# Kernel optimization log

Hardware: AMD Instinct MI355X
Metric: run time of the kernel (lower is better)

The kernel has to match this reference:

```python
import jax, jax.numpy as jnp
import numpy as np

HIDDEN_DIM = 64
VOCAB_SIZE = 64
NUM_SLOTS = 64
B, L = 256, 4096
EPS = 1e-5


def setup_inputs() -> dict:
    key = jax.random.key(0)
    ks = jax.random.split(key, 8)
    s = 0.02
    return {
        "seq": jax.random.randint(ks[0], (B, L), 0, VOCAB_SIZE),
        "embed": jax.random.normal(ks[1], (VOCAB_SIZE, HIDDEN_DIM), jnp.float32) * s,
        "W1": jax.random.normal(ks[2], (HIDDEN_DIM, 2 * HIDDEN_DIM), jnp.float32) * s,
        "b1": jnp.zeros((2 * HIDDEN_DIM,), jnp.float32),
        "W2": jax.random.normal(ks[3], (2 * HIDDEN_DIM, HIDDEN_DIM), jnp.float32) * s,
        "b2": jnp.zeros((HIDDEN_DIM,), jnp.float32),
        "gamma": jnp.ones((HIDDEN_DIM,), jnp.float32),
        "beta": jnp.zeros((HIDDEN_DIM,), jnp.float32),
        "Wq": jax.random.normal(ks[4], (HIDDEN_DIM, HIDDEN_DIM), jnp.float32) * s,
        "bq": jnp.zeros((HIDDEN_DIM,), jnp.float32),
        "Wo": jax.random.normal(ks[5], (HIDDEN_DIM, VOCAB_SIZE), jnp.float32) * s,
        "bo": jnp.zeros((VOCAB_SIZE,), jnp.float32),
    }


def reference(seq, embed, W1, b1, W2, b2, gamma, beta, Wq, bq, Wo, bo):
    # Encoder: embed -> FF residual -> LayerNorm
    e = embed[seq]                                   # [B, L, H]
    ff = jax.nn.relu(e @ W1 + b1) @ W2 + b2          # [B, L, H]
    h = e + ff
    mu = jnp.mean(h, axis=-1, keepdims=True)
    var = jnp.mean(jnp.square(h - mu), axis=-1, keepdims=True)
    hs = (h - mu) * jax.lax.rsqrt(var + EPS) * gamma + beta  # [B, L, H]

    # Top-k gating over content token norms
    content = hs[:, :-3, :]                          # [B, L-3, H]
    gate_scores = jnp.linalg.norm(content, axis=-1)  # [B, L-3]
    _, idx = jax.lax.top_k(gate_scores, NUM_SLOTS)   # [B, k], k == num_slots (L-3 >= k)
    slots = jnp.take_along_axis(content, idx[:, :, None], axis=1)  # [B, k, H]

    # Tiny single-query attention over gathered slots
    q = hs[:, -1, :] @ Wq + bq                       # [B, H]
    scores = jnp.einsum("bh,bkh->bk", q, slots) / jnp.sqrt(jnp.float32(HIDDEN_DIM))
    attn = jax.nn.softmax(scores, axis=-1)           # [B, k]
    ctx = jnp.einsum("bk,bkh->bh", attn, slots)      # [B, H]
    return ctx @ Wo + bo                             # [B, VOCAB]
```

## Files before the change

kernel.cpp:

```cpp
#include <hip/hip_runtime.h>
#include <math.h>

#define EPS 1e-5f


__global__ __launch_bounds__(512) void table_hist(
    const int* __restrict__ seq,
    const float* __restrict__ embed,
    const float* __restrict__ W1, const float* __restrict__ b1,
    const float* __restrict__ W2, const float* __restrict__ b2,
    const float* __restrict__ gamma, const float* __restrict__ beta,
    float* __restrict__ wsf, int* __restrict__ wsi_hist,
    int* __restrict__ wsi_tlast)
{
    const int tid = threadIdx.x;
    const int wv  = tid >> 6;
    const int ln  = tid & 63;

    if (blockIdx.x < 8) {
        const int t = blockIdx.x * 8 + wv;
        float e = embed[t * 64 + ln];

        float a0p0 = b1[ln],      a0p1 = 0.f;
        float a1p0 = b1[64 + ln], a1p1 = 0.f;
        #pragma unroll 8
        for (int j = 0; j < 64; j += 2) {
            float ej0 = __shfl(e, j);
            float ej1 = __shfl(e, j + 1);
            a0p0 = fmaf(ej0, W1[j * 128 + ln],            a0p0);
            a1p0 = fmaf(ej0, W1[j * 128 + 64 + ln],       a1p0);
            a0p1 = fmaf(ej1, (W1 + 128)[j * 128 + ln],      a0p1);
            a1p1 = fmaf(ej1, (W1 + 128)[j * 128 + 64 + ln], a1p1);
        }
        float u0 = fmaxf(a0p0 + a0p1, 0.f);
        float u1 = fmaxf(a1p0 + a1p1, 0.f);

        float hp0 = e + b2[ln], hp1 = 0.f;
        #pragma unroll 8
        for (int k = 0; k < 64; k += 2) {
            hp0 = fmaf(__shfl(u0, k),     W2[k * 64 + ln],       hp0);
            hp1 = fmaf(__shfl(u0, k + 1), W2[(k + 1) * 64 + ln], hp1);
        }
        #pragma unroll 8
        for (int k = 0; k < 64; k += 2) {
            hp0 = fmaf(__shfl(u1, k),     W2[(64 + k) * 64 + ln],     hp0);
            hp1 = fmaf(__shfl(u1, k + 1), W2[(64 + k + 1) * 64 + ln], hp1);
        }
        float h = hp0 + hp1;

        float s = h;
        #pragma unroll
        for (int off = 1; off < 64; off <<= 1) s += __shfl_xor(s, off);
        float mu = s * (1.f / 64.f);
        float d = h - mu;
        float v = d * d;
        #pragma unroll
        for (int off = 1; off < 64; off <<= 1) v += __shfl_xor(v, off);
        float rstd = rsqrtf(v * (1.f / 64.f) + EPS);
        float hs = d * rstd * gamma[ln] + beta[ln];
        wsf[t * 64 + ln] = hs;
        float ss = hs * hs;
        #pragma unroll
        for (int off = 1; off < 64; off <<= 1) ss += __shfl_xor(ss, off);
        if (ln == 0) wsf[4096 + t] = sqrtf(ss);
    } else {
        __shared__ int hist[8][64];
        const int b = blockIdx.x - 8;
        const int* row = seq + b * 4096;

        hist[wv][ln] = 0;
        int4 v0 = reinterpret_cast<const int4*>(row)[tid];
        int4 v1 = reinterpret_cast<const int4*>(row)[tid + 512];
        __syncthreads();

        atomicAdd(&hist[wv][v0.x], 1); atomicAdd(&hist[wv][v0.y], 1);
        atomicAdd(&hist[wv][v0.z], 1); atomicAdd(&hist[wv][v0.w], 1);
        atomicAdd(&hist[wv][v1.x], 1);
        if (tid != 511) {
            atomicAdd(&hist[wv][v1.y], 1);
            atomicAdd(&hist[wv][v1.z], 1);
            atomicAdd(&hist[wv][v1.w], 1);
        } else {
            wsi_tlast[b] = v1.w;
        }
        __syncthreads();

        if (tid < 64) {
            int hsum = 0;
            #pragma unroll
            for (int w = 0; w < 8; ++w) hsum += hist[w][tid];
            wsi_hist[b * 64 + tid] = hsum;
        }
    }
}

__global__ __launch_bounds__(256) void slot_epilogue(
    const float* __restrict__ Wq, const float* __restrict__ bq,
    const float* __restrict__ Wo, const float* __restrict__ bo,
    const float* __restrict__ wsf, const int* __restrict__ wsi_hist,
    const int* __restrict__ wsi_tlast,
    float* __restrict__ out)
{
    __shared__ float HS[64][65];
    __shared__ float qv[64];

    const int tid = threadIdx.x;
    const int wv  = tid >> 6;
    const int ln  = tid & 63;
    const int b   = blockIdx.x;

    float wcol[64];
    float bias = 0.f, sc_r = 0.f;
    int h = 0, tl = 0;
    if (wv == 0) {
        #pragma unroll
        for (int k = 0; k < 64; ++k) wcol[k] = Wo[k * 64 + ln];
        bias = bo[ln];
        sc_r = wsf[4096 + ln];
        h    = wsi_hist[b * 64 + ln];
    } else if (wv == 1) {
        #pragma unroll
        for (int k = 0; k < 64; ++k) wcol[k] = Wq[k * 64 + ln];
        bias = bq[ln];
        tl   = wsi_tlast[b];
    }

    #pragma unroll
    for (int i = 0; i < 4; ++i) {
        int idx4 = tid + 256 * i;
        float4 v = reinterpret_cast<const float4*>(wsf)[idx4];
        int t = idx4 >> 4, j0 = (idx4 & 15) << 2;
        HS[t][j0] = v.x; HS[t][j0+1] = v.y; HS[t][j0+2] = v.z; HS[t][j0+3] = v.w;
    }
    __syncthreads();

    int cnt_i = 0;
    if (wv == 0) {
        float my = sc_r;
        int S = 0;
        for (int t2 = 0; t2 < 64; ++t2) {
            float s2 = __shfl(sc_r, t2);
            int   h2 = __shfl(h, t2);
            bool before = (s2 > my) || (s2 == my && t2 < ln);
            if (before) S += h2;
        }
        int rem = 64 - S;
        rem = rem < 0 ? 0 : rem;
        cnt_i = h < rem ? h : rem;
    } else if (wv == 1) {
        float acc = bias;
        #pragma unroll
        for (int k = 0; k < 64; ++k)
            acc = fmaf(HS[tl][k], wcol[k], acc);
        qv[ln] = acc;
    }
    __syncthreads();

    if (wv == 0) {
        float acc = 0.f;
        #pragma unroll 8
        for (int k = 0; k < 64; ++k)
            acc = fmaf(qv[k], HS[ln][k], acc);
        float logit = acc * 0.125f;
        float lm = (cnt_i > 0) ? logit : -1e30f;
        #pragma unroll
        for (int off = 1; off < 64; off <<= 1) lm = fmaxf(lm, __shfl_xor(lm, off));
        float wvv = (cnt_i > 0) ? (float)cnt_i * __expf(logit - lm) : 0.f;
        float z = wvv;
        #pragma unroll
        for (int off = 1; off < 64; off <<= 1) z += __shfl_xor(z, off);
        float w_reg = wvv / z;

        float cacc = 0.f;
        #pragma unroll 8
        for (int t2 = 0; t2 < 64; ++t2)
            cacc = fmaf(__shfl(w_reg, t2), HS[t2][ln], cacc);

        float oacc = bias;
        #pragma unroll
        for (int k = 0; k < 64; ++k)
            oacc = fmaf(__shfl(cacc, k), wcol[k], oacc);
        out[b * 64 + ln] = oacc;
    }
}

extern "C" void kernel_launch(void* const* d_in, const int* in_sizes, int n_in,
                              void* d_out, int out_size, void* d_ws, size_t ws_size,
                              hipStream_t stream) {
    const int*   seq   = (const int*)d_in[0];
    const float* embed = (const float*)d_in[1];
    const float* W1    = (const float*)d_in[2];
    const float* b1    = (const float*)d_in[3];
    const float* W2    = (const float*)d_in[4];
    const float* b2    = (const float*)d_in[5];
    const float* gamma = (const float*)d_in[6];
    const float* beta  = (const float*)d_in[7];
    const float* Wq    = (const float*)d_in[8];
    const float* bq    = (const float*)d_in[9];
    const float* Wo    = (const float*)d_in[10];
    const float* bo    = (const float*)d_in[11];
    float* out = (float*)d_out;
    float* wsf = (float*)d_ws;
    int*   wsi_hist  = (int*)(wsf + 4160);
    int*   wsi_tlast = wsi_hist + 256 * 64;
    (void)in_sizes; (void)n_in; (void)out_size; (void)ws_size;

    table_hist<<<264, 512, 0, stream>>>(seq, embed, W1, b1, W2, b2,
                                        gamma, beta, wsf, wsi_hist, wsi_tlast);
    slot_epilogue<<<256, 256, 0, stream>>>(Wq, bq, Wo, bo, wsf, wsi_hist,
                                           wsi_tlast, out);
}
```

Before: 19.82 us.

## Halve table_hist block size, unroll loops, and drop one barrier in epilogue

The table/histogram kernel moves from 512-thread to 256-thread blocks, with 16 table blocks of 4 waves each and a 4-iteration strided loop for the histogram. The MLP loops are fully unrolled. In the epilogue, the query wave reads the last token's row straight from global memory and uses shuffles instead of shared memory, which lets one __syncthreads be removed. The aim is to cut barrier and latency overhead and spread the table work across more CUs, at the cost of extra registers from full unrolling.

```diff
diff --git a/kernel.cpp b/kernel.cpp
--- a/kernel.cpp
+++ b/kernel.cpp
@@ -4,7 +4,7 @@
 #define EPS 1e-5f
 
 
-__global__ __launch_bounds__(512) void table_hist(
+__global__ __launch_bounds__(256) void table_hist(
     const int* __restrict__ seq,
     const float* __restrict__ embed,
     const float* __restrict__ W1, const float* __restrict__ b1,
@@ -17,34 +17,34 @@
     const int wv  = tid >> 6;
     const int ln  = tid & 63;
 
-    if (blockIdx.x < 8) {
-        const int t = blockIdx.x * 8 + wv;
+    if (blockIdx.x < 16) {
+        const int t = blockIdx.x * 4 + wv;
         float e = embed[t * 64 + ln];
 
-        float a0p0 = b1[ln],      a0p1 = 0.f;
-        float a1p0 = b1[64 + ln], a1p1 = 0.f;
-        #pragma unroll 8
+        float a0 = b1[ln],      a0b = 0.f;
+        float a1 = b1[64 + ln], a1b = 0.f;
+        #pragma unroll
         for (int j = 0; j < 64; j += 2) {
             float ej0 = __shfl(e, j);
             float ej1 = __shfl(e, j + 1);
-            a0p0 = fmaf(ej0, W1[j * 128 + ln],            a0p0);
-            a1p0 = fmaf(ej0, W1[j * 128 + 64 + ln],       a1p0);
-            a0p1 = fmaf(ej1, (W1 + 128)[j * 128 + ln],      a0p1);
-            a1p1 = fmaf(ej1, (W1 + 128)[j * 128 + 64 + ln], a1p1);
-        }
-        float u0 = fmaxf(a0p0 + a0p1, 0.f);
-        float u1 = fmaxf(a1p0 + a1p1, 0.f);
+            a0  = fmaf(ej0, W1[j * 128 + ln],            a0);
+            a1  = fmaf(ej0, W1[j * 128 + 64 + ln],       a1);
+            a0b = fmaf(ej1, W1[(j + 1) * 128 + ln],      a0b);
+            a1b = fmaf(ej1, W1[(j + 1) * 128 + 64 + ln], a1b);
+        }
+        float u0 = fmaxf(a0 + a0b, 0.f);
+        float u1 = fmaxf(a1 + a1b, 0.f);
 
         float hp0 = e + b2[ln], hp1 = 0.f;
-        #pragma unroll 8
+        #pragma unroll
         for (int k = 0; k < 64; k += 2) {
             hp0 = fmaf(__shfl(u0, k),     W2[k * 64 + ln],       hp0);
             hp1 = fmaf(__shfl(u0, k + 1), W2[(k + 1) * 64 + ln], hp1);
         }
-        #pragma unroll 8
+        #pragma unroll
         for (int k = 0; k < 64; k += 2) {
-            hp0 = fmaf(__shfl(u1, k),     W2[(64 + k) * 64 + ln],     hp0);
-            hp1 = fmaf(__shfl(u1, k + 1), W2[(64 + k + 1) * 64 + ln], hp1);
+            hp0 = fmaf(__shfl(u1, k),     W2[(64 + k) * 64 + ln], hp0);
+            hp1 = fmaf(__shfl(u1, k + 1), W2[(65 + k) * 64 + ln], hp1);
         }
         float h = hp0 + hp1;
 
@@ -64,33 +64,33 @@
         for (int off = 1; off < 64; off <<= 1) ss += __shfl_xor(ss, off);
         if (ln == 0) wsf[4096 + t] = sqrtf(ss);
     } else {
-        __shared__ int hist[8][64];
-        const int b = blockIdx.x - 8;
+        __shared__ int hist[4][64];
+        const int b = blockIdx.x - 16;
         const int* row = seq + b * 4096;
 
         hist[wv][ln] = 0;
-        int4 v0 = reinterpret_cast<const int4*>(row)[tid];
-        int4 v1 = reinterpret_cast<const int4*>(row)[tid + 512];
         __syncthreads();
 
-        atomicAdd(&hist[wv][v0.x], 1); atomicAdd(&hist[wv][v0.y], 1);
-        atomicAdd(&hist[wv][v0.z], 1); atomicAdd(&hist[wv][v0.w], 1);
-        atomicAdd(&hist[wv][v1.x], 1);
-        if (tid != 511) {
-            atomicAdd(&hist[wv][v1.y], 1);
-            atomicAdd(&hist[wv][v1.z], 1);
-            atomicAdd(&hist[wv][v1.w], 1);
-        } else {
-            wsi_tlast[b] = v1.w;
+        #pragma unroll
+        for (int i = 0; i < 4; ++i) {
+            int idx = tid + 256 * i;
+            if (idx < 1023) {
+                int4 v = reinterpret_cast<const int4*>(row)[idx];
+                atomicAdd(&hist[wv][v.x], 1);
+                atomicAdd(&hist[wv][v.y], 1);
+                atomicAdd(&hist[wv][v.z], 1);
+                atomicAdd(&hist[wv][v.w], 1);
+            }
+        }
+        if (tid == 0) {
+            atomicAdd(&hist[0][row[4092]], 1);
+            wsi_tlast[b] = row[4095];
         }
         __syncthreads();
 
-        if (tid < 64) {
-            int hsum = 0;
-            #pragma unroll
-            for (int w = 0; w < 8; ++w) hsum += hist[w][tid];
-            wsi_hist[b * 64 + tid] = hsum;
-        }
+        if (tid < 64)
+            wsi_hist[b * 64 + tid] =
+                hist[0][tid] + hist[1][tid] + hist[2][tid] + hist[3][tid];
     }
 }
 
@@ -110,8 +110,8 @@
     const int b   = blockIdx.x;
 
     float wcol[64];
-    float bias = 0.f, sc_r = 0.f;
-    int h = 0, tl = 0;
+    float bias = 0.f, sc_r = 0.f, hsq = 0.f;
+    int h = 0;
     if (wv == 0) {
         #pragma unroll
         for (int k = 0; k < 64; ++k) wcol[k] = Wo[k * 64 + ln];
@@ -122,7 +122,8 @@
         #pragma unroll
         for (int k = 0; k < 64; ++k) wcol[k] = Wq[k * 64 + ln];
         bias = bq[ln];
-        tl   = wsi_tlast[b];
+        int tl = wsi_tlast[b];
+        hsq  = wsf[tl * 64 + ln];
     }
 
     #pragma unroll
@@ -132,12 +133,12 @@
         int t = idx4 >> 4, j0 = (idx4 & 15) << 2;
         HS[t][j0] = v.x; HS[t][j0+1] = v.y; HS[t][j0+2] = v.z; HS[t][j0+3] = v.w;
     }
-    __syncthreads();
 
     int cnt_i = 0;
     if (wv == 0) {
         float my = sc_r;
         int S = 0;
+        #pragma unroll
         for (int t2 = 0; t2 < 64; ++t2) {
             float s2 = __shfl(sc_r, t2);
             int   h2 = __shfl(h, t2);
@@ -151,7 +152,7 @@
         float acc = bias;
         #pragma unroll
         for (int k = 0; k < 64; ++k)
-            acc = fmaf(HS[tl][k], wcol[k], acc);
+            acc = fmaf(__shfl(hsq, k), wcol[k], acc);
         qv[ln] = acc;
     }
     __syncthreads();
@@ -205,7 +206,7 @@
     int*   wsi_tlast = wsi_hist + 256 * 64;
     (void)in_sizes; (void)n_in; (void)out_size; (void)ws_size;
 
-    table_hist<<<264, 512, 0, stream>>>(seq, embed, W1, b1, W2, b2,
+    table_hist<<<272, 256, 0, stream>>>(seq, embed, W1, b1, W2, b2,
                                         gamma, beta, wsf, wsi_hist, wsi_tlast);
     slot_epilogue<<<256, 256, 0, stream>>>(Wq, bq, Wo, bo, wsf, wsi_hist,
                                            wsi_tlast, out);
```

Measured after the change: 18.82 us. 5.0% less time.
